# Kernel optimization log

Hardware: AMD Instinct MI355X
Metric: run time of the kernel (lower is better)

## Reference

```python
import jax, jax.numpy as jnp
import numpy as np

N = 50000   # number of 'link' nodes
E = 800000  # edges per relation
H = 64      # h_dim

def setup_inputs() -> dict:
    key = jax.random.key(0)
    ks = jax.random.split(key, 9)
    return dict(
        h=jax.random.normal(ks[0], (N, H), jnp.float32),
        feat1=jax.random.normal(ks[1], (E, H), jnp.float32),
        feat2=jax.random.normal(ks[2], (E, H), jnp.float32),
        W1=jax.random.normal(ks[3], (2 * H, H), jnp.float32) / np.sqrt(2.0 * H).astype(np.float32),
        b1=jnp.zeros((H,), jnp.float32),
        W2=jax.random.normal(ks[4], (2 * H, H), jnp.float32) / np.sqrt(2.0 * H).astype(np.float32),
        b2=jnp.zeros((H,), jnp.float32),
        src1=jax.random.randint(ks[5], (E,), 0, N, jnp.int32),
        dst1=jax.random.randint(ks[6], (E,), 0, N, jnp.int32),
        src2=jax.random.randint(ks[7], (E,), 0, N, jnp.int32),
        dst2=jax.random.randint(ks[8], (E,), 0, N, jnp.int32),
    )

def _agg(h, src, dst, feat):
    # e_mul_u: edge feat * source node h, then sum-reduce to destination nodes
    return jax.ops.segment_sum(feat * h[src], dst, num_segments=N)

def reference(h, feat1, feat2, W1, b1, W2, b2, src1, dst1, src2, dst2):
    # n_layer = 2 message-passing steps, each with its own Linear(2H, H)
    for W, b in ((W1, b1), (W2, b2)):
        a1 = _agg(h, src1, dst1, feat1)          # [N, H] connect_to aggregate
        a2 = _agg(h, src2, dst2, feat2)          # [N, H] connected_by aggregate
        h_ = jnp.concatenate([a1, a2], axis=-1)  # cross-reducer concat -> [N, 2H]
        h_ = jax.nn.relu(h_ @ W + b)             # Linear + ReLU
        h = h + h_                               # residual update
    return h
```

## Files before the change

kernel.cpp:

```cpp
#include <hip/hip_runtime.h>

#define N_NODES 50000
#define HDIM 64
#define E_EDGES 800000
#define SCAN_T 1024


__global__ void __launch_bounds__(256) hist_kernel(
        const int* __restrict__ dst1, const int* __restrict__ dst2,
        int* __restrict__ cnt1, int* __restrict__ cnt2) {
    const int* dst = blockIdx.y ? dst2 : dst1;
    int* cnt       = blockIdx.y ? cnt2 : cnt1;
    int e = blockIdx.x * 256 + threadIdx.x;
    if (e < E_EDGES) atomicAdd(&cnt[dst[e]], 1);
}

__global__ void __launch_bounds__(SCAN_T) scan_kernel(
        const int* __restrict__ cnt1, const int* __restrict__ cnt2,
        int* __restrict__ off1, int* __restrict__ off2,
        int* __restrict__ cur1, int* __restrict__ cur2) {
    const int* cnt = blockIdx.x ? cnt2 : cnt1;
    int* off       = blockIdx.x ? off2 : off1;
    int* cur       = blockIdx.x ? cur2 : cur1;

    __shared__ int lds[SCAN_T];
    const int t = threadIdx.x;
    const int chunk = (N_NODES + SCAN_T - 1) / SCAN_T;
    const int beg = t * chunk;
    const int end = min(beg + chunk, N_NODES);

    int sum = 0;
    for (int i = beg; i < end; ++i) sum += cnt[i];
    lds[t] = sum;
    __syncthreads();

    for (int s = 1; s < SCAN_T; s <<= 1) {
        int v = (t >= s) ? lds[t - s] : 0;
        __syncthreads();
        lds[t] += v;
        __syncthreads();
    }

    int run = lds[t] - sum;
    for (int i = beg; i < end; ++i) {
        off[i] = run;
        cur[i] = run;
        run += cnt[i];
    }
    if (t == SCAN_T - 1) off[N_NODES] = lds[SCAN_T - 1];
}

__global__ void __launch_bounds__(256) scatter_kernel(
        const int* __restrict__ src1, const int* __restrict__ dst1,
        const int* __restrict__ src2, const int* __restrict__ dst2,
        int* __restrict__ cur1, int* __restrict__ cur2,
        int2* __restrict__ pairs1, int2* __restrict__ pairs2) {
    const int* src = blockIdx.y ? src2 : src1;
    const int* dst = blockIdx.y ? dst2 : dst1;
    int* cur       = blockIdx.y ? cur2 : cur1;
    int2* pairs    = blockIdx.y ? pairs2 : pairs1;
    int e = blockIdx.x * 256 + threadIdx.x;
    if (e >= E_EDGES) return;
    int pos = atomicAdd(&cur[dst[e]], 1);
    pairs[pos] = make_int2(src[e], e);
}


__global__ void __launch_bounds__(256) agg_csr_kernel(
        const float* __restrict__ h,
        const float* __restrict__ feat1, const float* __restrict__ feat2,
        const int* __restrict__ off1, const int* __restrict__ off2,
        const int2* __restrict__ pairs1, const int2* __restrict__ pairs2,
        float* __restrict__ a1, float* __restrict__ a2) {
    const float* feat  = blockIdx.y ? feat2  : feat1;
    const int* off     = blockIdx.y ? off2   : off1;
    const int2* pairs  = blockIdx.y ? pairs2 : pairs1;
    float* agg         = blockIdx.y ? a2     : a1;

    const int tid  = threadIdx.x;
    const int lane = tid & 63;
    const int g    = lane >> 4;
    const int q    = lane & 15;
    const int node = blockIdx.x * 4 + (tid >> 6);
    if (node >= N_NODES) return;

    const int beg = off[node];
    const int end = off[node + 1];

    float4 acc = make_float4(0.f, 0.f, 0.f, 0.f);
    int i = beg + g;
    if (i < end) {
        int2 p = pairs[i];
        for (; i + 4 < end; i += 4) {
            int2 pn = pairs[i + 4];
            const float4 f  = *(const float4*)&feat[(size_t)p.y * HDIM + q * 4];
            const float4 hv = *(const float4*)&h[(size_t)p.x * HDIM + q * 4];
            acc.x = fmaf(f.x, hv.x, acc.x);
            acc.y = fmaf(f.y, hv.y, acc.y);
            acc.z = fmaf(f.z, hv.z, acc.z);
            acc.w = fmaf(f.w, hv.w, acc.w);
            p = pn;
        }
        const float4 f  = *(const float4*)&feat[(size_t)p.y * HDIM + q * 4];
        const float4 hv = *(const float4*)&h[(size_t)p.x * HDIM + q * 4];
        acc.x = fmaf(f.x, hv.x, acc.x);
        acc.y = fmaf(f.y, hv.y, acc.y);
        acc.z = fmaf(f.z, hv.z, acc.z);
        acc.w = fmaf(f.w, hv.w, acc.w);
    }

    acc.x += __shfl_xor(acc.x, 16); acc.y += __shfl_xor(acc.y, 16);
    acc.z += __shfl_xor(acc.z, 16); acc.w += __shfl_xor(acc.w, 16);
    acc.x += __shfl_xor(acc.x, 32); acc.y += __shfl_xor(acc.y, 32);
    acc.z += __shfl_xor(acc.z, 32); acc.w += __shfl_xor(acc.w, 32);

    if (lane < 16) {
        *(float4*)&agg[(size_t)node * HDIM + q * 4] = acc;
    }
}


__global__ void __launch_bounds__(256) mlp_kernel(
        const float* __restrict__ h_in,
        const float* __restrict__ a1,
        const float* __restrict__ a2,
        const float* __restrict__ W,
        const float* __restrict__ b,
        float* __restrict__ h_out) {
    __shared__ float Wlds[2 * HDIM * HDIM];

    const int tid = threadIdx.x;
    for (int i = tid * 4; i < 2 * HDIM * HDIM; i += 256 * 4) {
        *(float4*)&Wlds[i] = *(const float4*)&W[i];
    }
    __syncthreads();

    const int lane = tid & 63;
    const int stride = gridDim.x * 4;
    for (int node = blockIdx.x * 4 + (tid >> 6); node < N_NODES; node += stride) {
        const size_t base = (size_t)node * HDIM;
        const float x1 = a1[base + lane];
        const float x2 = a2[base + lane];

        float acc = b[lane];
#pragma unroll
        for (int k = 0; k < HDIM; ++k)
            acc = fmaf(__shfl(x1, k), Wlds[k * HDIM + lane], acc);
#pragma unroll
        for (int k = 0; k < HDIM; ++k)
            acc = fmaf(__shfl(x2, k), Wlds[(HDIM + k) * HDIM + lane], acc);

        h_out[base + lane] = h_in[base + lane] + fmaxf(acc, 0.0f);
    }
}


__global__ void __launch_bounds__(256) agg_atomic_kernel(
        const float* __restrict__ h,
        const float* __restrict__ feat,
        const int* __restrict__ src,
        const int* __restrict__ dst,
        float* __restrict__ agg) {
    const int tid  = blockIdx.x * 256 + threadIdx.x;
    const int lane = threadIdx.x & 63;
    const int sub  = lane >> 4;
    const int q    = lane & 15;
    const int e    = (tid >> 6) * 4 + sub;
    if (e >= E_EDGES) return;
    const int s = src[e];
    const int d = dst[e];
    const float4 f  = *(const float4*)&feat[(size_t)e * HDIM + q * 4];
    const float4 hv = *(const float4*)&h[(size_t)s * HDIM + q * 4];
    float* p = &agg[(size_t)d * HDIM + q * 4];
    atomicAdd(p + 0, f.x * hv.x);
    atomicAdd(p + 1, f.y * hv.y);
    atomicAdd(p + 2, f.z * hv.z);
    atomicAdd(p + 3, f.w * hv.w);
}

extern "C" void kernel_launch(void* const* d_in, const int* in_sizes, int n_in,
                              void* d_out, int out_size, void* d_ws, size_t ws_size,
                              hipStream_t stream) {
    const float* h     = (const float*)d_in[0];
    const float* feat1 = (const float*)d_in[1];
    const float* feat2 = (const float*)d_in[2];
    const float* W1    = (const float*)d_in[3];
    const float* b1    = (const float*)d_in[4];
    const float* W2    = (const float*)d_in[5];
    const float* b2    = (const float*)d_in[6];
    const int*   src1  = (const int*)d_in[7];
    const int*   dst1  = (const int*)d_in[8];
    const int*   src2  = (const int*)d_in[9];
    const int*   dst2  = (const int*)d_in[10];

    float* out = (float*)d_out;

    float* a1   = (float*)d_ws;
    float* a2   = a1 + (size_t)N_NODES * HDIM;
    int*   cnt1 = (int*)(a2 + (size_t)N_NODES * HDIM);
    int*   cnt2 = cnt1 + N_NODES;
    int*   off1 = cnt2 + N_NODES;
    int*   off2 = off1 + (N_NODES + 1);
    int*   cur1 = off2 + (N_NODES + 1);
    int*   cur2 = cur1 + N_NODES;
    int2*  pairs1 = (int2*)(cur2 + N_NODES);
    int2*  pairs2 = pairs1 + E_EDGES;

    const size_t needed = (char*)(pairs2 + E_EDGES) - (char*)d_ws;

    const int eBlocks   = (E_EDGES + 255) / 256;
    const int nBlocks   = (N_NODES + 3) / 4;

    if (ws_size >= needed) {
        hipMemsetAsync(cnt1, 0, 2 * (size_t)N_NODES * sizeof(int), stream);
        hist_kernel<<<dim3(eBlocks, 2), 256, 0, stream>>>(dst1, dst2, cnt1, cnt2);
        scan_kernel<<<2, SCAN_T, 0, stream>>>(cnt1, cnt2, off1, off2, cur1, cur2);
        scatter_kernel<<<dim3(eBlocks, 2), 256, 0, stream>>>(
            src1, dst1, src2, dst2, cur1, cur2, pairs1, pairs2);

        agg_csr_kernel<<<dim3(nBlocks, 2), 256, 0, stream>>>(
            h, feat1, feat2, off1, off2, pairs1, pairs2, a1, a2);
        mlp_kernel<<<1024, 256, 0, stream>>>(h, a1, a2, W1, b1, out);

        agg_csr_kernel<<<dim3(nBlocks, 2), 256, 0, stream>>>(
            out, feat1, feat2, off1, off2, pairs1, pairs2, a1, a2);
        mlp_kernel<<<1024, 256, 0, stream>>>(out, a1, a2, W2, b2, out);
    } else {
        const size_t aggBytes = 2 * (size_t)N_NODES * HDIM * sizeof(float);
        const int atomBlocks = (E_EDGES + 15) / 16;

        hipMemsetAsync(d_ws, 0, aggBytes, stream);
        agg_atomic_kernel<<<atomBlocks, 256, 0, stream>>>(h, feat1, src1, dst1, a1);
        agg_atomic_kernel<<<atomBlocks, 256, 0, stream>>>(h, feat2, src2, dst2, a2);
        mlp_kernel<<<1024, 256, 0, stream>>>(h, a1, a2, W1, b1, out);

        hipMemsetAsync(d_ws, 0, aggBytes, stream);
        agg_atomic_kernel<<<atomBlocks, 256, 0, stream>>>(out, feat1, src1, dst1, a1);
        agg_atomic_kernel<<<atomBlocks, 256, 0, stream>>>(out, feat2, src2, dst2, a2);
        mlp_kernel<<<1024, 256, 0, stream>>>(out, a1, a2, W2, b2, out);
    }
}
```

Measured before the change: 1.002 ms.

## Parallelize CSR scan, use edge-chunked segment aggregation, register-resident MLP weights

Replaces the two-block serial scan with a three-stage multi-block scan: per-block partial sums, a scan of those partials, then a fill pass. The aggregation kernel now gives each wave a fixed chunk of 128 edges and finds the nodes that start in that chunk by binary search. Lanes map to hidden features and read edge indices with readfirstlane. The MLP keeps the weight columns in registers, broadcasts inputs with readlane instead of using LDS, and sets launch bounds to 2 blocks per CU. The goals are to remove the serial scan bottleneck, balance aggregation work across edges rather than nodes, and cut LDS traffic in the MLP. The costs are higher register pressure and extra binary-search reads.

After: 890.6 us. 11.2% less time.

```diff
diff --git a/kernel.cpp b/kernel.cpp
--- a/kernel.cpp
+++ b/kernel.cpp
@@ -3,7 +3,14 @@
 #define N_NODES 50000
 #define HDIM 64
 #define E_EDGES 800000
-#define SCAN_T 1024
+#define SCAN_BLK 1024
+#define NPART ((N_NODES + SCAN_BLK - 1) / SCAN_BLK)
+#define CHUNK 128
+#define SEG_WAVES ((E_EDGES + CHUNK - 1) / CHUNK)
+
+__device__ __forceinline__ float lane_bcast(float v, int l) {
+    return __int_as_float(__builtin_amdgcn_readlane(__float_as_int(v), l));
+}
 
 
 __global__ void __launch_bounds__(256) hist_kernel(
@@ -15,39 +22,63 @@
     if (e < E_EDGES) atomicAdd(&cnt[dst[e]], 1);
 }
 
-__global__ void __launch_bounds__(SCAN_T) scan_kernel(
+__global__ void __launch_bounds__(SCAN_BLK) partial_kernel(
         const int* __restrict__ cnt1, const int* __restrict__ cnt2,
+        int* __restrict__ part) {
+    const int* cnt = blockIdx.y ? cnt2 : cnt1;
+    __shared__ int red[16];
+    const int t = blockIdx.x * SCAN_BLK + threadIdx.x;
+    int v = (t < N_NODES) ? cnt[t] : 0;
+#pragma unroll
+    for (int s = 32; s >= 1; s >>= 1) v += __shfl_xor(v, s);
+    if ((threadIdx.x & 63) == 0) red[threadIdx.x >> 6] = v;
+    __syncthreads();
+    if (threadIdx.x == 0) {
+        int ssum = 0;
+#pragma unroll
+        for (int i = 0; i < 16; ++i) ssum += red[i];
+        part[blockIdx.y * NPART + blockIdx.x] = ssum;
+    }
+}
+
+__global__ void __launch_bounds__(64) scanp_kernel(
+        const int* __restrict__ part, int* __restrict__ pofs) {
+    const int r = blockIdx.y;
+    const int t = threadIdx.x;
+    int v = (t < NPART) ? part[r * NPART + t] : 0;
+    const int orig = v;
+#pragma unroll
+    for (int s = 1; s < 64; s <<= 1) {
+        int u = __shfl_up(v, s);
+        if (t >= s) v += u;
+    }
+    if (t < NPART) pofs[r * NPART + t] = v - orig;
+}
+
+__global__ void __launch_bounds__(SCAN_BLK) fill_kernel(
+        const int* __restrict__ cnt1, const int* __restrict__ cnt2,
+        const int* __restrict__ pofs,
         int* __restrict__ off1, int* __restrict__ off2,
         int* __restrict__ cur1, int* __restrict__ cur2) {
-    const int* cnt = blockIdx.x ? cnt2 : cnt1;
-    int* off       = blockIdx.x ? off2 : off1;
-    int* cur       = blockIdx.x ? cur2 : cur1;
-
-    __shared__ int lds[SCAN_T];
+    const int* cnt = blockIdx.y ? cnt2 : cnt1;
+    int* off       = blockIdx.y ? off2 : off1;
+    int* cur       = blockIdx.y ? cur2 : cur1;
+
+    __shared__ int lds[SCAN_BLK];
     const int t = threadIdx.x;
-    const int chunk = (N_NODES + SCAN_T - 1) / SCAN_T;
-    const int beg = t * chunk;
-    const int end = min(beg + chunk, N_NODES);
-
-    int sum = 0;
-    for (int i = beg; i < end; ++i) sum += cnt[i];
-    lds[t] = sum;
+    const int gid = blockIdx.x * SCAN_BLK + t;
+    const int c = (gid < N_NODES) ? cnt[gid] : 0;
+    lds[t] = c;
     __syncthreads();
-
-    for (int s = 1; s < SCAN_T; s <<= 1) {
+    for (int s = 1; s < SCAN_BLK; s <<= 1) {
         int v = (t >= s) ? lds[t - s] : 0;
         __syncthreads();
         lds[t] += v;
         __syncthreads();
     }
-
-    int run = lds[t] - sum;
-    for (int i = beg; i < end; ++i) {
-        off[i] = run;
-        cur[i] = run;
-        run += cnt[i];
-    }
-    if (t == SCAN_T - 1) off[N_NODES] = lds[SCAN_T - 1];
+    const int excl = lds[t] - c + pofs[blockIdx.y * NPART + blockIdx.x];
+    if (gid < N_NODES) { off[gid] = excl; cur[gid] = excl; }
+    if (gid == 0 && blockIdx.x == 0) off[N_NODES] = E_EDGES;
 }
 
 __global__ void __launch_bounds__(256) scatter_kernel(
@@ -66,91 +97,99 @@
 }
 
 
-__global__ void __launch_bounds__(256) agg_csr_kernel(
+__global__ void __launch_bounds__(256) agg_seg_kernel(
         const float* __restrict__ h,
         const float* __restrict__ feat1, const float* __restrict__ feat2,
         const int* __restrict__ off1, const int* __restrict__ off2,
         const int2* __restrict__ pairs1, const int2* __restrict__ pairs2,
         float* __restrict__ a1, float* __restrict__ a2) {
-    const float* feat  = blockIdx.y ? feat2  : feat1;
-    const int* off     = blockIdx.y ? off2   : off1;
-    const int2* pairs  = blockIdx.y ? pairs2 : pairs1;
-    float* agg         = blockIdx.y ? a2     : a1;
-
-    const int tid  = threadIdx.x;
-    const int lane = tid & 63;
-    const int g    = lane >> 4;
-    const int q    = lane & 15;
-    const int node = blockIdx.x * 4 + (tid >> 6);
-    if (node >= N_NODES) return;
-
-    const int beg = off[node];
-    const int end = off[node + 1];
-
-    float4 acc = make_float4(0.f, 0.f, 0.f, 0.f);
-    int i = beg + g;
-    if (i < end) {
-        int2 p = pairs[i];
-        for (; i + 4 < end; i += 4) {
-            int2 pn = pairs[i + 4];
-            const float4 f  = *(const float4*)&feat[(size_t)p.y * HDIM + q * 4];
-            const float4 hv = *(const float4*)&h[(size_t)p.x * HDIM + q * 4];
-            acc.x = fmaf(f.x, hv.x, acc.x);
-            acc.y = fmaf(f.y, hv.y, acc.y);
-            acc.z = fmaf(f.z, hv.z, acc.z);
-            acc.w = fmaf(f.w, hv.w, acc.w);
-            p = pn;
+    const float* feat = blockIdx.y ? feat2  : feat1;
+    const int* off    = blockIdx.y ? off2   : off1;
+    const int2* pairs = blockIdx.y ? pairs2 : pairs1;
+    float* agg        = blockIdx.y ? a2     : a1;
+
+    const int lane = threadIdx.x & 63;
+    const int wv = blockIdx.x * 4 + (threadIdx.x >> 6);
+    if (wv >= SEG_WAVES) return;
+
+    const int C0 = wv * CHUNK;
+    int C1 = C0 + CHUNK;
+    if (C1 >= E_EDGES) C1 = E_EDGES + 1;
+
+    int lo = 0, hi = N_NODES;
+    while (lo < hi) {
+        int mid = (lo + hi) >> 1;
+        if (off[mid] < C0) lo = mid + 1; else hi = mid;
+    }
+    int n = lo;
+    if (n >= N_NODES) return;
+
+    int s = off[n];
+    while (s >= C0 && s < C1) {
+        const int e = off[n + 1];
+        float acc = 0.f;
+        int i = s;
+        for (; i + 4 <= e; i += 4) {
+            int2 p0 = pairs[i];
+            int2 p1 = pairs[i + 1];
+            int2 p2 = pairs[i + 2];
+            int2 p3 = pairs[i + 3];
+            const float f0 = feat[((size_t)__builtin_amdgcn_readfirstlane(p0.y) << 6) + lane];
+            const float g0 = h   [((size_t)__builtin_amdgcn_readfirstlane(p0.x) << 6) + lane];
+            const float f1 = feat[((size_t)__builtin_amdgcn_readfirstlane(p1.y) << 6) + lane];
+            const float g1 = h   [((size_t)__builtin_amdgcn_readfirstlane(p1.x) << 6) + lane];
+            const float f2 = feat[((size_t)__builtin_amdgcn_readfirstlane(p2.y) << 6) + lane];
+            const float g2 = h   [((size_t)__builtin_amdgcn_readfirstlane(p2.x) << 6) + lane];
+            const float f3 = feat[((size_t)__builtin_amdgcn_readfirstlane(p3.y) << 6) + lane];
+            const float g3 = h   [((size_t)__builtin_amdgcn_readfirstlane(p3.x) << 6) + lane];
+            acc = fmaf(f0, g0, acc);
+            acc = fmaf(f1, g1, acc);
+            acc = fmaf(f2, g2, acc);
+            acc = fmaf(f3, g3, acc);
         }
-        const float4 f  = *(const float4*)&feat[(size_t)p.y * HDIM + q * 4];
-        const float4 hv = *(const float4*)&h[(size_t)p.x * HDIM + q * 4];
-        acc.x = fmaf(f.x, hv.x, acc.x);
-        acc.y = fmaf(f.y, hv.y, acc.y);
-        acc.z = fmaf(f.z, hv.z, acc.z);
-        acc.w = fmaf(f.w, hv.w, acc.w);
-    }
-
-    acc.x += __shfl_xor(acc.x, 16); acc.y += __shfl_xor(acc.y, 16);
-    acc.z += __shfl_xor(acc.z, 16); acc.w += __shfl_xor(acc.w, 16);
-    acc.x += __shfl_xor(acc.x, 32); acc.y += __shfl_xor(acc.y, 32);
-    acc.z += __shfl_xor(acc.z, 32); acc.w += __shfl_xor(acc.w, 32);
-
-    if (lane < 16) {
-        *(float4*)&agg[(size_t)node * HDIM + q * 4] = acc;
-    }
-}
-
-
-__global__ void __launch_bounds__(256) mlp_kernel(
+        for (; i < e; ++i) {
+            int2 p = pairs[i];
+            const float f = feat[((size_t)__builtin_amdgcn_readfirstlane(p.y) << 6) + lane];
+            const float g = h   [((size_t)__builtin_amdgcn_readfirstlane(p.x) << 6) + lane];
+            acc = fmaf(f, g, acc);
+        }
+        agg[((size_t)n << 6) + lane] = acc;
+        if (++n >= N_NODES) break;
+        s = e;
+    }
+}
+
+
+__global__ void __launch_bounds__(256, 2) mlp_kernel(
         const float* __restrict__ h_in,
         const float* __restrict__ a1,
         const float* __restrict__ a2,
         const float* __restrict__ W,
         const float* __restrict__ b,
         float* __restrict__ h_out) {
-    __shared__ float Wlds[2 * HDIM * HDIM];
-
-    const int tid = threadIdx.x;
-    for (int i = tid * 4; i < 2 * HDIM * HDIM; i += 256 * 4) {
-        *(float4*)&Wlds[i] = *(const float4*)&W[i];
-    }
-    __syncthreads();
-
-    const int lane = tid & 63;
+    const int lane = threadIdx.x & 63;
+
+    float w1r[HDIM], w2r[HDIM];
+#pragma unroll
+    for (int k = 0; k < HDIM; ++k) w1r[k] = W[k * HDIM + lane];
+#pragma unroll
+    for (int k = 0; k < HDIM; ++k) w2r[k] = W[(HDIM + k) * HDIM + lane];
+    const float bias = b[lane];
+
+    const int wv = blockIdx.x * 4 + (threadIdx.x >> 6);
     const int stride = gridDim.x * 4;
-    for (int node = blockIdx.x * 4 + (tid >> 6); node < N_NODES; node += stride) {
-        const size_t base = (size_t)node * HDIM;
+    for (int node = wv; node < N_NODES; node += stride) {
+        const size_t base = (size_t)node << 6;
         const float x1 = a1[base + lane];
         const float x2 = a2[base + lane];
-
-        float acc = b[lane];
-#pragma unroll
-        for (int k = 0; k < HDIM; ++k)
-            acc = fmaf(__shfl(x1, k), Wlds[k * HDIM + lane], acc);
-#pragma unroll
-        for (int k = 0; k < HDIM; ++k)
-            acc = fmaf(__shfl(x2, k), Wlds[(HDIM + k) * HDIM + lane], acc);
-
-        h_out[base + lane] = h_in[base + lane] + fmaxf(acc, 0.0f);
+        float acc1 = bias, acc2 = 0.f;
+#pragma unroll
+        for (int k = 0; k < HDIM; ++k) {
+            acc1 = fmaf(lane_bcast(x1, k), w1r[k], acc1);
+            acc2 = fmaf(lane_bcast(x2, k), w2r[k], acc2);
+        }
+        const float r = acc1 + acc2;
+        h_out[base + lane] = h_in[base + lane] + fmaxf(r, 0.f);
     }
 }
 
@@ -203,26 +242,31 @@
     int*   off2 = off1 + (N_NODES + 1);
     int*   cur1 = off2 + (N_NODES + 1);
     int*   cur2 = cur1 + N_NODES;
-    int2*  pairs1 = (int2*)(cur2 + N_NODES);
+    int*   part = cur2 + N_NODES;
+    int*   pofs = part + 2 * NPART;
+    int2*  pairs1 = (int2*)(pofs + 2 * NPART);
     int2*  pairs2 = pairs1 + E_EDGES;
 
     const size_t needed = (char*)(pairs2 + E_EDGES) - (char*)d_ws;
 
     const int eBlocks   = (E_EDGES + 255) / 256;
-    const int nBlocks   = (N_NODES + 3) / 4;
+    const int segBlocks = (SEG_WAVES + 3) / 4;
 
     if (ws_size >= needed) {
         hipMemsetAsync(cnt1, 0, 2 * (size_t)N_NODES * sizeof(int), stream);
         hist_kernel<<<dim3(eBlocks, 2), 256, 0, stream>>>(dst1, dst2, cnt1, cnt2);
-        scan_kernel<<<2, SCAN_T, 0, stream>>>(cnt1, cnt2, off1, off2, cur1, cur2);
+        partial_kernel<<<dim3(NPART, 2), SCAN_BLK, 0, stream>>>(cnt1, cnt2, part);
+        scanp_kernel<<<dim3(1, 2), 64, 0, stream>>>(part, pofs);
+        fill_kernel<<<dim3(NPART, 2), SCAN_BLK, 0, stream>>>(
+            cnt1, cnt2, pofs, off1, off2, cur1, cur2);
         scatter_kernel<<<dim3(eBlocks, 2), 256, 0, stream>>>(
             src1, dst1, src2, dst2, cur1, cur2, pairs1, pairs2);
 
-        agg_csr_kernel<<<dim3(nBlocks, 2), 256, 0, stream>>>(
+        agg_seg_kernel<<<dim3(segBlocks, 2), 256, 0, stream>>>(
             h, feat1, feat2, off1, off2, pairs1, pairs2, a1, a2);
         mlp_kernel<<<1024, 256, 0, stream>>>(h, a1, a2, W1, b1, out);
 
-        agg_csr_kernel<<<dim3(nBlocks, 2), 256, 0, stream>>>(
+        agg_seg_kernel<<<dim3(segBlocks, 2), 256, 0, stream>>>(
             out, feat1, feat2, off1, off2, pairs1, pairs2, a1, a2);
         mlp_kernel<<<1024, 256, 0, stream>>>(out, a1, a2, W2, b2, out);
     } else {
```
